# Kernel optimization log

Measured on AMD Instinct MI355X. Metric: run time of the kernel, lower is better.

The kernel has to match this reference:

```python
import jax, jax.numpy as jnp
import numpy as np

B, L, DM = 2, 2048, 2048
EXP = 2; DI = EXP * DM          # d_inner = 4096
N = 64                           # d_state
K = 4                            # d_conv
P = 64                           # headdim
H = DI // P                      # n_heads = 64
G = 1                            # n_groups
CONV = DI + 2 * G * N            # 4224
PROJ = 2 * DI + 2 * G * N + H    # 8384
EPS = 1e-6


def setup_inputs() -> dict:
    ks = jax.random.split(jax.random.key(0), 6)
    s = 0.02
    return {
        'u': jax.random.normal(ks[0], (B, L, DM), jnp.float32),
        'ln_w': jnp.ones((DM,), jnp.float32),
        'in_proj_w': jax.random.normal(ks[1], (PROJ, DM), jnp.float32) * s,
        'conv_w': jax.random.normal(ks[2], (K, CONV), jnp.float32) * 0.1,
        'conv_b': jnp.zeros((CONV,), jnp.float32),
        'dt_bias': jax.random.uniform(ks[3], (H,), jnp.float32, 0.0, 1.0),
        'A_log': jnp.log(jnp.arange(1, H + 1, dtype=jnp.float32)),
        'D': jnp.ones((H,), jnp.float32),
        'norm_w': jnp.ones((DI,), jnp.float32),
        'out_proj_w': jax.random.normal(ks[4], (DM, DI), jnp.float32) * s,
    }


def _rmsnorm(x, w, eps=EPS):
    xf = x.astype(jnp.float32)
    v = jnp.mean(xf * xf, axis=-1, keepdims=True)
    return w * (xf * jax.lax.rsqrt(v + eps)).astype(x.dtype)


def reference(u, ln_w, in_proj_w, conv_w, conv_b, dt_bias, A_log, D, norm_w, out_proj_w):
    residual = u
    hs = _rmsnorm(u, ln_w)                                 # input RMSNorm
    zxbcdt = hs @ in_proj_w.T                              # (B,L,PROJ)
    z, xBC, dt = jnp.split(zxbcdt, [DI, DI + CONV], axis=-1)
    # causal depthwise conv1d over time + SiLU
    xp = jnp.pad(xBC, ((0, 0), (K - 1, 0), (0, 0)))
    xc = conv_b + sum(xp[:, k:k + L, :] * conv_w[k] for k in range(K))
    xc = jax.nn.silu(xc)
    x, Bm, Cm = jnp.split(xc, [DI, DI + G * N], axis=-1)
    x = x.reshape(B, L, H, P)
    Bm = jnp.repeat(Bm.reshape(B, L, G, N), H // G, axis=2)  # (B,L,H,N)
    Cm = jnp.repeat(Cm.reshape(B, L, G, N), H // G, axis=2)
    dt = jax.nn.softplus(dt + dt_bias)                       # (B,L,H)
    dA = jnp.exp(dt * (-jnp.exp(A_log)))                     # (B,L,H)
    dtx = dt[..., None] * x                                  # (B,L,H,P)

    def step(h, inp):
        dA_t, dtx_t, B_t, C_t = inp
        # h: (B,H,P,N); h_t = exp(dt*A) h_{t-1} + (dt*x_t) outer B_t
        h = dA_t[:, :, None, None] * h + dtx_t[..., None] * B_t[:, :, None, :]
        y = jnp.einsum('bhpn,bhn->bhp', h, C_t)
        return h, y

    h0 = jnp.zeros((B, H, P, N), jnp.float32)
    _, ys = jax.lax.scan(step, h0, (dA.transpose(1, 0, 2),
                                    dtx.transpose(1, 0, 2, 3),
                                    Bm.transpose(1, 0, 2, 3),
                                    Cm.transpose(1, 0, 2, 3)))
    y = ys.transpose(1, 0, 2, 3) + D[None, None, :, None] * x   # (B,L,H,P)
    # gated RMSNorm: (y * silu(z)) -> rmsnorm
    y = _rmsnorm(y.reshape(B, L, DI) * jax.nn.silu(z), norm_w)
    out = y @ out_proj_w.T
    return residual + out
```

## Files before the change

kernel.cpp:

```cpp
#include <hip/hip_runtime.h>
#include <hip/hip_bf16.h>

typedef __bf16 bf16;
typedef __bf16 bf16x8 __attribute__((ext_vector_type(8)));
typedef float f32x4 __attribute__((ext_vector_type(4)));

#define B_    2
#define L_    2048
#define DM_   2048
#define DI_   4096
#define NST   64
#define PD    64
#define NH    64
#define CONV_ 4224
#define XBCD_ 4288
#define PROJ_ 8384
#define BL_   (B_ * L_)
#define NCHUNK 32
#define EPS_  1e-6f

#define WAITV(n) asm volatile("s_waitcnt vmcnt(" #n ")" ::: "memory")
#define BAR()    __builtin_amdgcn_s_barrier()

__device__ __forceinline__ float block_reduce_sum_256(float v) {
  #pragma unroll
  for (int m = 32; m; m >>= 1) v += __shfl_xor(v, m, 64);
  __shared__ float sred[4];
  int w = threadIdx.x >> 6;
  if ((threadIdx.x & 63) == 0) sred[w] = v;
  __syncthreads();
  return sred[0] + sred[1] + sred[2] + sred[3];
}

__device__ __forceinline__ float silu_f(float x) {
  return x / (1.0f + expf(-x));
}

__device__ __forceinline__ void async16(const bf16* g, bf16* l) {
  __builtin_amdgcn_global_load_lds(
      (__attribute__((address_space(1))) void*)g,
      (__attribute__((address_space(3))) void*)l, 16, 0, 0);
}

__global__ __launch_bounds__(256) void rmsnorm_in_kernel(
    const float* __restrict__ u, const float* __restrict__ w, bf16* __restrict__ hs) {
  int row = blockIdx.x;
  const float* x = u + (size_t)row * DM_;
  int base = threadIdx.x * 8;
  f32x4 v0 = *(const f32x4*)(x + base);
  f32x4 v1 = *(const f32x4*)(x + base + 4);
  float xv[8], ss = 0.f;
  #pragma unroll
  for (int i = 0; i < 4; i++) { xv[i] = v0[i]; xv[4 + i] = v1[i]; }
  #pragma unroll
  for (int i = 0; i < 8; i++) ss += xv[i] * xv[i];
  ss = block_reduce_sum_256(ss);
  float r = rsqrtf(ss / (float)DM_ + EPS_);
  f32x4 w0 = *(const f32x4*)(w + base);
  f32x4 w1 = *(const f32x4*)(w + base + 4);
  bf16x8 o;
  #pragma unroll
  for (int i = 0; i < 4; i++) { o[i] = (bf16)(w0[i] * xv[i] * r); o[4 + i] = (bf16)(w1[i] * xv[4 + i] * r); }
  *(bf16x8*)(hs + (size_t)row * DM_ + base) = o;
}

__global__ __launch_bounds__(256) void convert_w_kernel(
    const float* __restrict__ src, bf16* __restrict__ dst,
    long n_src, long n_dst) {
  long e = ((long)blockIdx.x * 256 + threadIdx.x) * 8;
  if (e >= n_dst) return;
  bf16x8 o;
  if (e < n_src) {
    f32x4 a = *(const f32x4*)(src + e);
    f32x4 b = *(const f32x4*)(src + e + 4);
    #pragma unroll
    for (int q = 0; q < 4; q++) { o[q] = (bf16)a[q]; o[4 + q] = (bf16)b[q]; }
  } else {
    #pragma unroll
    for (int q = 0; q < 8; q++) o[q] = (bf16)0.f;
  }
  *(bf16x8*)(dst + e) = o;
}

template <bool OUT_F32>
__global__ __launch_bounds__(256, 2) void gemm_nt_db(
    const bf16* __restrict__ A, int lda,
    const bf16* __restrict__ W, int ldw,
    void* __restrict__ Cout, int ldc, const float* __restrict__ resid,
    int N, int K) {
  __shared__ __align__(16) bf16 As[2][128 * 64];
  __shared__ __align__(16) bf16 Bs[2][128 * 64];
  int nwg = gridDim.x * gridDim.y;
  int bid = blockIdx.y * gridDim.x + blockIdx.x;
  int q8 = nwg >> 3, r8 = nwg & 7;
  int xcd = bid & 7, loc = bid >> 3;
  int nb = (xcd < r8 ? xcd * (q8 + 1) : r8 * (q8 + 1) + (xcd - r8) * q8) + loc;
  int bn = nb % gridDim.x, bm = nb / gridDim.x;
  int m0 = bm * 128, n0 = bn * 128;
  int tid = threadIdx.x, wave = tid >> 6, lane = tid & 63;
  int wm = (wave >> 1) * 64, wn = (wave & 1) * 64;
  int lm = lane & 15, lk = (lane >> 4) * 8;
  int lr = lane >> 3;
  int cse = ((lane & 7) ^ lr) * 8;
  f32x4 acc[4][4] = {};

  auto stage = [&](int d, int t) {
    #pragma unroll
    for (int i = 0; i < 4; ++i) {
      int row = (wave * 4 + i) * 8;
      async16(A + (size_t)(m0 + row + lr) * lda + t * 64 + cse, &As[d][row * 64]);
      async16(W + (size_t)(n0 + row + lr) * ldw + t * 64 + cse, &Bs[d][row * 64]);
    }
  };

  int NT = K / 64;
  stage(0, 0);
  for (int t = 0; t < NT; ++t) {
    int d = t & 1;
    if (t + 1 < NT) { stage(d ^ 1, t + 1); WAITV(8); }
    else            { WAITV(0); }
    BAR();
    #pragma unroll
    for (int ks = 0; ks < 64; ks += 32) {
      bf16x8 af[4], bf[4];
      #pragma unroll
      for (int i = 0; i < 4; ++i) {
        int row = wm + i * 16 + lm;
        af[i] = *(const bf16x8*)&As[d][row * 64 + ((((ks + lk) >> 3) ^ (row & 7)) << 3)];
      }
      #pragma unroll
      for (int j = 0; j < 4; ++j) {
        int row = wn + j * 16 + lm;
        bf[j] = *(const bf16x8*)&Bs[d][row * 64 + ((((ks + lk) >> 3) ^ (row & 7)) << 3)];
      }
      #pragma unroll
      for (int i = 0; i < 4; ++i)
        #pragma unroll
        for (int j = 0; j < 4; ++j)
          acc[i][j] = __builtin_amdgcn_mfma_f32_16x16x32_bf16(af[i], bf[j], acc[i][j], 0, 0, 0);
    }
    BAR();
  }
  int r0 = m0 + wm + (lane >> 4) * 4;
  #pragma unroll
  for (int i = 0; i < 4; ++i) {
    #pragma unroll
    for (int j = 0; j < 4; ++j) {
      int col = n0 + wn + j * 16 + lm;
      if (col < N) {
        #pragma unroll
        for (int r = 0; r < 4; ++r) {
          int row = r0 + i * 16 + r;
          size_t idx = (size_t)row * ldc + col;
          float v = acc[i][j][r];
          if (resid) v += resid[idx];
          if (OUT_F32) ((float*)Cout)[idx] = v;
          else         ((bf16*)Cout)[idx]  = (bf16)v;
        }
      }
    }
  }
}

__global__ __launch_bounds__(256) void conv_bc_kernel(
    const bf16* __restrict__ xbcdt, const float* __restrict__ cw,
    const float* __restrict__ cb, bf16* __restrict__ xc) {
  int idx = blockIdx.x * 256 + threadIdx.x;
  if (idx >= BL_ * 16) return;
  int c8 = idx & 15, t = idx >> 4;
  int l = t % L_;
  int c = DI_ + c8 * 8;
  float acc[8];
  f32x4 bv0 = *(const f32x4*)(cb + c);
  f32x4 bv1 = *(const f32x4*)(cb + c + 4);
  #pragma unroll
  for (int q = 0; q < 4; q++) { acc[q] = bv0[q]; acc[4 + q] = bv1[q]; }
  #pragma unroll
  for (int k = 0; k < 4; k++) {
    int ls = l + k - 3;
    if (ls >= 0) {
      const bf16* xp = xbcdt + (size_t)(t + k - 3) * XBCD_ + c;
      bf16x8 xv = *(const bf16x8*)xp;
      f32x4 wv0 = *(const f32x4*)(cw + k * CONV_ + c);
      f32x4 wv1 = *(const f32x4*)(cw + k * CONV_ + c + 4);
      #pragma unroll
      for (int q = 0; q < 4; q++) { acc[q] += (float)xv[q] * wv0[q]; acc[4 + q] += (float)xv[4 + q] * wv1[q]; }
    }
  }
  bf16x8 o;
  #pragma unroll
  for (int q = 0; q < 8; q++) o[q] = (bf16)silu_f(acc[q]);
  *(bf16x8*)(xc + (size_t)t * CONV_ + c) = o;
}

__global__ __launch_bounds__(256) void dt_kernel(
    const bf16* __restrict__ xbcdt, const float* __restrict__ dt_bias,
    float* __restrict__ dtH) {
  int idx = blockIdx.x * 256 + threadIdx.x;
  if (idx >= BL_ * NH) return;
  int h = idx & 63, t = idx >> 6;
  float raw = (float)xbcdt[(size_t)t * XBCD_ + CONV_ + h] + dt_bias[h];
  float v = (raw > 20.f) ? raw : log1pf(expf(raw));
  dtH[(size_t)h * BL_ + t] = v;
}

__global__ __launch_bounds__(256) void scan_chunk_mfma(
    bf16* __restrict__ xc, const bf16* __restrict__ xbcdt,
    const float* __restrict__ cw, const float* __restrict__ cb,
    const float* __restrict__ dtH,
    const float* __restrict__ A_log, const float* __restrict__ Dp,
    bf16* __restrict__ Sc) {
  __shared__ bf16 Bs[64][72];
  __shared__ bf16 Cs[64][72];
  __shared__ bf16 Xt[64][72];
  __shared__ bf16 Gh[64][72];
  __shared__ bf16 Gl[64][72];
  __shared__ float dts[64];
  __shared__ float cum[64];
  __shared__ float wsA[64];
  int bi = blockIdx.x;
  int h = bi & 63, c = (bi >> 6) & 31, b = bi >> 11;
  int tid = threadIdx.x;
  int wave = tid >> 6, lane = tid & 63;
  int lm = lane & 15, lk = (lane >> 4) * 8;
  int cl = lane & 15, rw4 = (lane >> 4) * 4;
  int wt = (wave >> 1) * 32, wq = (wave & 1) * 32;
  size_t rowbase = (size_t)b * L_ + c * 64;
  float aA = expf(A_log[h]);
  #pragma unroll
  for (int i = 0; i < 2; i++) {
    int cc = tid + i * 256;
    int s = cc >> 3, e8 = (cc & 7) * 8;
    const bf16* base = xc + (rowbase + s) * CONV_;
    bf16x8 bv = *(const bf16x8*)(base + DI_ + e8);
    bf16x8 cv = *(const bf16x8*)(base + DI_ + NST + e8);
    *(bf16x8*)&Bs[s][e8 ^ (s & 56)] = bv;
    *(bf16x8*)&Cs[s][e8] = cv;
    int col = h * PD + e8;
    int l = c * 64 + s;
    float acc[8];
    f32x4 cb0 = *(const f32x4*)(cb + col);
    f32x4 cb1 = *(const f32x4*)(cb + col + 4);
    #pragma unroll
    for (int q = 0; q < 4; q++) { acc[q] = cb0[q]; acc[4 + q] = cb1[q]; }
    #pragma unroll
    for (int k = 0; k < 4; k++) {
      int ls = l + k - 3;
      if (ls >= 0) {
        const bf16* xp = xbcdt + (rowbase + s + k - 3) * XBCD_ + col;
        bf16x8 xv = *(const bf16x8*)xp;
        f32x4 wv0 = *(const f32x4*)(cw + k * CONV_ + col);
        f32x4 wv1 = *(const f32x4*)(cw + k * CONV_ + col + 4);
        #pragma unroll
        for (int q = 0; q < 4; q++) { acc[q] += (float)xv[q] * wv0[q]; acc[4 + q] += (float)xv[4 + q] * wv1[q]; }
      }
    }
    #pragma unroll
    for (int q = 0; q < 8; q++) Xt[e8 + q][s ^ e8] = (bf16)silu_f(acc[q]);
  }
  if (tid < 64) dts[tid] = dtH[(size_t)h * BL_ + rowbase + tid];
  __syncthreads();
  if (tid < 64) {
    float v = dts[tid];
    #pragma unroll
    for (int off = 1; off < 64; off <<= 1) {
      float o = __shfl_up(v, off, 64);
      if (tid >= off) v += o;
    }
    cum[tid] = v;
  }
  __syncthreads();
  if (tid < 64) wsA[tid] = expf(-aA * (cum[63] - cum[tid])) * dts[tid];
  f32x4 gacc[2][2] = {};
  #pragma unroll
  for (int ks = 0; ks < 64; ks += 32) {
    bf16x8 af[2], bfr[2];
    #pragma unroll
    for (int i = 0; i < 2; i++) af[i] = *(bf16x8*)&Cs[wt + i * 16 + lm][ks + lk];
    #pragma unroll
    for (int j = 0; j < 2; j++) {
      int S = wq + j * 16 + lm;
      bfr[j] = *(bf16x8*)&Bs[S][(ks + lk) ^ (S & 56)];
    }
    #pragma unroll
    for (int i = 0; i < 2; i++)
      #pragma unroll
      for (int j = 0; j < 2; j++)
        gacc[i][j] = __builtin_amdgcn_mfma_f32_16x16x32_bf16(af[i], bfr[j], gacc[i][j], 0, 0, 0);
  }
  #pragma unroll
  for (int i = 0; i < 2; i++) {
    #pragma unroll
    for (int j = 0; j < 2; j++) {
      #pragma unroll
      for (int r = 0; r < 4; r++) {
        int t = wt + i * 16 + rw4 + r;
        int s = wq + j * 16 + cl;
        float g = 0.f;
        if (s <= t) g = gacc[i][j][r] * expf(-aA * (cum[t] - cum[s])) * dts[s];
        bf16 ghi = (bf16)g;
        Gh[t][s] = ghi;
        Gl[t][s] = (bf16)(g - (float)ghi);
      }
    }
  }
  __syncthreads();
  f32x4 yacc[2][2] = {};
  #pragma unroll
  for (int ks = 0; ks < 64; ks += 32) {
    bf16x8 ah[2], al[2], bx[2];
    #pragma unroll
    for (int i = 0; i < 2; i++) {
      ah[i] = *(bf16x8*)&Gh[wt + i * 16 + lm][ks + lk];
      al[i] = *(bf16x8*)&Gl[wt + i * 16 + lm][ks + lk];
    }
    #pragma unroll
    for (int j = 0; j < 2; j++) {
      int P = wq + j * 16 + lm;
      bx[j] = *(bf16x8*)&Xt[P][(ks + lk) ^ (P & 56)];
    }
    #pragma unroll
    for (int i = 0; i < 2; i++)
      #pragma unroll
      for (int j = 0; j < 2; j++) {
        yacc[i][j] = __builtin_amdgcn_mfma_f32_16x16x32_bf16(ah[i], bx[j], yacc[i][j], 0, 0, 0);
        yacc[i][j] = __builtin_amdgcn_mfma_f32_16x16x32_bf16(al[i], bx[j], yacc[i][j], 0, 0, 0);
      }
  }
  float Dv = Dp[h];
  #pragma unroll
  for (int i = 0; i < 2; i++) {
    #pragma unroll
    for (int j = 0; j < 2; j++) {
      int p = wq + j * 16 + cl;
      #pragma unroll
      for (int r = 0; r < 4; r++) {
        int t = wt + i * 16 + rw4 + r;
        float yv = yacc[i][j][r] + Dv * (float)Xt[p][t ^ (p & 56)];
        xc[(rowbase + t) * CONV_ + h * PD + p] = (bf16)yv;
      }
    }
  }
  __syncthreads();
  #pragma unroll
  for (int i = 0; i < 2; i++) {
    int cc = tid + i * 256;
    int n = cc >> 3, s8 = (cc & 7) * 8;
    bf16x8 vh, vl;
    #pragma unroll
    for (int q = 0; q < 8; q++) {
      int s = s8 + q;
      float wb = (float)Bs[s][n ^ (s & 56)] * wsA[s];
      vh[q] = (bf16)wb;
      vl[q] = (bf16)(wb - (float)vh[q]);
    }
    *(bf16x8*)&Gh[n][s8] = vh;
    *(bf16x8*)&Gl[n][s8] = vl;
  }
  __syncthreads();
  f32x4 sacc[2][2] = {};
  #pragma unroll
  for (int ks = 0; ks < 64; ks += 32) {
    bf16x8 ax[2], bh[2], bl[2];
    #pragma unroll
    for (int i = 0; i < 2; i++) {
      int P = wt + i * 16 + lm;
      ax[i] = *(bf16x8*)&Xt[P][(ks + lk) ^ (P & 56)];
    }
    #pragma unroll
    for (int j = 0; j < 2; j++) {
      bh[j] = *(bf16x8*)&Gh[wq + j * 16 + lm][ks + lk];
      bl[j] = *(bf16x8*)&Gl[wq + j * 16 + lm][ks + lk];
    }
    #pragma unroll
    for (int i = 0; i < 2; i++)
      #pragma unroll
      for (int j = 0; j < 2; j++) {
        sacc[i][j] = __builtin_amdgcn_mfma_f32_16x16x32_bf16(ax[i], bh[j], sacc[i][j], 0, 0, 0);
        sacc[i][j] = __builtin_amdgcn_mfma_f32_16x16x32_bf16(ax[i], bl[j], sacc[i][j], 0, 0, 0);
      }
  }
  bf16* scp = Sc + ((((size_t)b * NCHUNK + c) * NH + h) << 12);
  #pragma unroll
  for (int i = 0; i < 2; i++) {
    #pragma unroll
    for (int j = 0; j < 2; j++) {
      int n = wq + j * 16 + cl;
      #pragma unroll
      for (int r = 0; r < 4; r++) {
        int p = wt + i * 16 + rw4 + r;
        scp[p * 64 + n] = (bf16)sacc[i][j][r];
      }
    }
  }
}

__global__ __launch_bounds__(256) void state_scan_kernel(
    bf16* __restrict__ Sc, const float* __restrict__ dtH,
    const float* __restrict__ A_log) {
  __shared__ float sdts[64];
  int b = blockIdx.x >> 6, h = blockIdx.x & 63;
  int tid = threadIdx.x;
  float aA = expf(A_log[h]);
  float H[16] = {};
  for (int c = 0; c < NCHUNK; c++) {
    if (tid < 64) sdts[tid] = dtH[(size_t)h * BL_ + b * L_ + c * 64 + tid];
    __syncthreads();
    float sum = 0.f;
    #pragma unroll 8
    for (int i = 0; i < 64; i++) sum += sdts[i];
    float Atot = expf(-aA * sum);
    bf16* p = Sc + ((((size_t)b * NCHUNK + c) * NH + h) << 12) + tid * 16;
    bf16x8 s0 = *(bf16x8*)p;
    bf16x8 s1 = *(bf16x8*)(p + 8);
    bf16x8 o0, o1;
    #pragma unroll
    for (int q = 0; q < 8; q++) {
      float n0 = Atot * H[q]     + (float)s0[q];
      float n1 = Atot * H[8 + q] + (float)s1[q];
      o0[q] = (bf16)H[q]; o1[q] = (bf16)H[8 + q];
      H[q] = n0; H[8 + q] = n1;
    }
    *(bf16x8*)p = o0;
    *(bf16x8*)(p + 8) = o1;
    __syncthreads();
  }
}

__global__ __launch_bounds__(256) void y_inter_mfma(
    bf16* __restrict__ xc, const float* __restrict__ dtH,
    const float* __restrict__ A_log, const bf16* __restrict__ Sc) {
  __shared__ bf16 Cs[64][72];
  __shared__ bf16 Hs[64][72];
  __shared__ float dts[64];
  __shared__ float eA[64];
  int bi = blockIdx.x;
  int h = bi & 63, c = (bi >> 6) & 31, b = bi >> 11;
  int tid = threadIdx.x;
  int wave = tid >> 6, lane = tid & 63;
  int lm = lane & 15, lk = (lane >> 4) * 8;
  int cl = lane & 15, rw4 = (lane >> 4) * 4;
  int wt = (wave >> 1) * 32, wp = (wave & 1) * 32;
  size_t rowbase = (size_t)b * L_ + c * 64;
  float aA = expf(A_log[h]);
  const bf16* scp = Sc + ((((size_t)b * NCHUNK + c) * NH + h) << 12);
  #pragma unroll
  for (int i = 0; i < 2; i++) {
    int cc = tid + i * 256;
    int s = cc >> 3, e8 = (cc & 7) * 8;
    bf16x8 cv = *(const bf16x8*)(xc + (rowbase + s) * CONV_ + DI_ + NST + e8);
    *(bf16x8*)&Cs[s][e8] = cv;
  }
  {
    int p = tid >> 2, n16 = (tid & 3) * 16;
    *(bf16x8*)&Hs[p][n16]     = *(const bf16x8*)(scp + p * 64 + n16);
    *(bf16x8*)&Hs[p][n16 + 8] = *(const bf16x8*)(scp + p * 64 + n16 + 8);
  }
  if (tid < 64) dts[tid] = dtH[(size_t)h * BL_ + rowbase + tid];
  __syncthreads();
  if (tid < 64) {
    float v = dts[tid];
    #pragma unroll
    for (int off = 1; off < 64; off <<= 1) {
      float o = __shfl_up(v, off, 64);
      if (tid >= off) v += o;
    }
    eA[tid] = expf(-aA * v);
  }
  __syncthreads();
  f32x4 acc[2][2] = {};
  #pragma unroll
  for (int ks = 0; ks < 64; ks += 32) {
    bf16x8 af[2], bfr[2];
    #pragma unroll
    for (int i = 0; i < 2; i++) af[i]  = *(bf16x8*)&Cs[wt + i * 16 + lm][ks + lk];
    #pragma unroll
    for (int j = 0; j < 2; j++) bfr[j] = *(bf16x8*)&Hs[wp + j * 16 + lm][ks + lk];
    #pragma unroll
    for (int i = 0; i < 2; i++)
      #pragma unroll
      for (int j = 0; j < 2; j++)
        acc[i][j] = __builtin_amdgcn_mfma_f32_16x16x32_bf16(af[i], bfr[j], acc[i][j], 0, 0, 0);
  }
  #pragma unroll
  for (int i = 0; i < 2; i++) {
    #pragma unroll
    for (int j = 0; j < 2; j++) {
      int p = wp + j * 16 + cl;
      #pragma unroll
      for (int r = 0; r < 4; r++) {
        int t = wt + i * 16 + rw4 + r;
        size_t gi = (rowbase + t) * CONV_ + h * PD + p;
        xc[gi] = (bf16)((float)xc[gi] + eA[t] * acc[i][j][r]);
      }
    }
  }
}

__global__ __launch_bounds__(256) void gated_norm_kernel(
    const bf16* __restrict__ xc, bf16* __restrict__ zbuf,
    const float* __restrict__ nw) {
  int t = blockIdx.x;
  int base = threadIdx.x * 16;
  const bf16* yr = xc + (size_t)t * CONV_;
  bf16* zr = zbuf + (size_t)t * DI_;
  float tv[16], ss = 0.f;
  #pragma unroll
  for (int i8 = 0; i8 < 2; i8++) {
    bf16x8 yv = *(const bf16x8*)(yr + base + i8 * 8);
    bf16x8 zv = *(const bf16x8*)(zr + base + i8 * 8);
    #pragma unroll
    for (int q = 0; q < 8; q++) {
      float tt = (float)yv[q] * silu_f((float)zv[q]);
      tv[i8 * 8 + q] = tt;
      ss += tt * tt;
    }
  }
  ss = block_reduce_sum_256(ss);
  float r = rsqrtf(ss / (float)DI_ + EPS_);
  #pragma unroll
  for (int i8 = 0; i8 < 2; i8++) {
    f32x4 w0 = *(const f32x4*)(nw + base + i8 * 8);
    f32x4 w1 = *(const f32x4*)(nw + base + i8 * 8 + 4);
    bf16x8 o;
    #pragma unroll
    for (int q = 0; q < 4; q++) {
      o[q]     = (bf16)(w0[q] * tv[i8 * 8 + q] * r);
      o[4 + q] = (bf16)(w1[q] * tv[i8 * 8 + 4 + q] * r);
    }
    *(bf16x8*)(zr + base + i8 * 8) = o;
  }
}

__global__ void ws_report_kernel(float* out, float ws_mb) {
  if (blockIdx.x == 0 && threadIdx.x == 0) out[0] = ws_mb;
}

extern "C" void kernel_launch(void* const* d_in, const int* in_sizes, int n_in,
                              void* d_out, int out_size, void* d_ws, size_t ws_size,
                              hipStream_t stream) {
  const float* u        = (const float*)d_in[0];
  const float* ln_w     = (const float*)d_in[1];
  const float* in_proj  = (const float*)d_in[2];
  const float* conv_w   = (const float*)d_in[3];
  const float* conv_b   = (const float*)d_in[4];
  const float* dt_bias  = (const float*)d_in[5];
  const float* A_log    = (const float*)d_in[6];
  const float* Dp       = (const float*)d_in[7];
  const float* norm_w   = (const float*)d_in[8];
  const float* out_proj = (const float*)d_in[9];
  float* out = (float*)d_out;

  bf16* hs = (bf16*)d_out;

  char* ws = (char*)d_ws;
  size_t off = 0;
  auto alloc = [&](size_t bytes) { char* p = ws + off; off = (off + bytes + 255) & ~(size_t)255; return p; };
  float* dtH  = (float*)alloc((size_t)BL_ * NH * 4);
  bf16*  wbuf = (bf16*)alloc((size_t)4352 * DM_ * 2);
  bf16*  shbuf= (bf16*)alloc((size_t)BL_ * XBCD_ * 2);
  bf16*  xc   = (bf16*)alloc((size_t)BL_ * CONV_ * 2);
  size_t need = off;

  if (ws_size < need) {
    ws_report_kernel<<<1, 64, 0, stream>>>(out, (float)(ws_size >> 20));
    return;
  }

  bf16* xbcdt = shbuf;
  bf16* zbuf  = shbuf;
  bf16* Sc = (bf16*)alloc((size_t)B_ * NCHUNK * NH * 64 * 64 * 2);
  need = off;
  if (ws_size < need) {
    ws_report_kernel<<<1, 64, 0, stream>>>(out, (float)(ws_size >> 20));
    return;
  }

  rmsnorm_in_kernel<<<BL_, 256, 0, stream>>>(u, ln_w, hs);

  {
    long nsrc = (long)XBCD_ * DM_, ndst = (long)4352 * DM_;
    convert_w_kernel<<<(int)(ndst / 8 / 256), 256, 0, stream>>>(
        in_proj + (size_t)DI_ * DM_, wbuf, nsrc, ndst);
    gemm_nt_db<false><<<dim3(4352 / 128, BL_ / 128), 256, 0, stream>>>(
        hs, DM_, wbuf, DM_, xbcdt, XBCD_, nullptr, XBCD_, DM_);
  }
  conv_bc_kernel<<<(BL_ * 16 + 255) / 256, 256, 0, stream>>>(
      xbcdt, conv_w, conv_b, xc);
  dt_kernel<<<(BL_ * NH + 255) / 256, 256, 0, stream>>>(
      xbcdt, dt_bias, dtH);
  scan_chunk_mfma<<<B_ * NH * NCHUNK, 256, 0, stream>>>(
      xc, xbcdt, conv_w, conv_b, dtH, A_log, Dp, Sc);
  state_scan_kernel<<<B_ * NH, 256, 0, stream>>>(Sc, dtH, A_log);
  y_inter_mfma<<<B_ * NH * NCHUNK, 256, 0, stream>>>(xc, dtH, A_log, Sc);

  {
    long n = (long)DI_ * DM_;
    convert_w_kernel<<<(int)(n / 8 / 256), 256, 0, stream>>>(in_proj, wbuf, n, n);
    gemm_nt_db<false><<<dim3(DI_ / 128, BL_ / 128), 256, 0, stream>>>(
        hs, DM_, wbuf, DM_, zbuf, DI_, nullptr, DI_, DM_);
  }
  gated_norm_kernel<<<BL_, 256, 0, stream>>>(xc, zbuf, norm_w);

  {
    long n = (long)DM_ * DI_;
    convert_w_kernel<<<(int)(n / 8 / 256), 256, 0, stream>>>(out_proj, wbuf, n, n);
    gemm_nt_db<true><<<dim3(DM_ / 128, BL_ / 128), 256, 0, stream>>>(
        zbuf, DI_, wbuf, DI_, out, DM_, u, DM_, DI_);
  }
}
```

Measured before the change: 599.2 us.

## Single-buffer GEMM for higher occupancy and parallelize inter-chunk state scan

The GEMM drops its double-buffered LDS staging for a single buffer, halving LDS use and raising the launch-bounds occupancy hint to 4 blocks per CU. Latency is now meant to be hidden by more resident workgroups rather than by prefetching. Separately, the per-chunk decay totals are precomputed in a new small kernel, and the state scan is split into 16x more blocks with one state element per thread. This replaces 128 serial blocks with a wide grid and coalesced strided accesses. The GEMM change risks exposing load latency if occupancy does not actually rise.

```diff
diff --git a/kernel.cpp b/kernel.cpp
--- a/kernel.cpp
+++ b/kernel.cpp
@@ -83,13 +83,13 @@
 }
 
 template <bool OUT_F32>
-__global__ __launch_bounds__(256, 2) void gemm_nt_db(
+__global__ __launch_bounds__(256, 4) void gemm_nt_sb(
     const bf16* __restrict__ A, int lda,
     const bf16* __restrict__ W, int ldw,
     void* __restrict__ Cout, int ldc, const float* __restrict__ resid,
     int N, int K) {
-  __shared__ __align__(16) bf16 As[2][128 * 64];
-  __shared__ __align__(16) bf16 Bs[2][128 * 64];
+  __shared__ __align__(16) bf16 As[128 * 64];
+  __shared__ __align__(16) bf16 Bs[128 * 64];
   int nwg = gridDim.x * gridDim.y;
   int bid = blockIdx.y * gridDim.x + blockIdx.x;
   int q8 = nwg >> 3, r8 = nwg & 7;
@@ -104,21 +104,15 @@
   int cse = ((lane & 7) ^ lr) * 8;
   f32x4 acc[4][4] = {};
 
-  auto stage = [&](int d, int t) {
+  int NT = K / 64;
+  for (int t = 0; t < NT; ++t) {
     #pragma unroll
     for (int i = 0; i < 4; ++i) {
       int row = (wave * 4 + i) * 8;
-      async16(A + (size_t)(m0 + row + lr) * lda + t * 64 + cse, &As[d][row * 64]);
-      async16(W + (size_t)(n0 + row + lr) * ldw + t * 64 + cse, &Bs[d][row * 64]);
-    }
-  };
-
-  int NT = K / 64;
-  stage(0, 0);
-  for (int t = 0; t < NT; ++t) {
-    int d = t & 1;
-    if (t + 1 < NT) { stage(d ^ 1, t + 1); WAITV(8); }
-    else            { WAITV(0); }
+      async16(A + (size_t)(m0 + row + lr) * lda + t * 64 + cse, &As[row * 64]);
+      async16(W + (size_t)(n0 + row + lr) * ldw + t * 64 + cse, &Bs[row * 64]);
+    }
+    WAITV(0);
     BAR();
     #pragma unroll
     for (int ks = 0; ks < 64; ks += 32) {
@@ -126,12 +120,12 @@
       #pragma unroll
       for (int i = 0; i < 4; ++i) {
         int row = wm + i * 16 + lm;
-        af[i] = *(const bf16x8*)&As[d][row * 64 + ((((ks + lk) >> 3) ^ (row & 7)) << 3)];
+        af[i] = *(const bf16x8*)&As[row * 64 + ((((ks + lk) >> 3) ^ (row & 7)) << 3)];
       }
       #pragma unroll
       for (int j = 0; j < 4; ++j) {
         int row = wn + j * 16 + lm;
-        bf[j] = *(const bf16x8*)&Bs[d][row * 64 + ((((ks + lk) >> 3) ^ (row & 7)) << 3)];
+        bf[j] = *(const bf16x8*)&Bs[row * 64 + ((((ks + lk) >> 3) ^ (row & 7)) << 3)];
       }
       #pragma unroll
       for (int i = 0; i < 4; ++i)
@@ -202,6 +196,20 @@
   float raw = (float)xbcdt[(size_t)t * XBCD_ + CONV_ + h] + dt_bias[h];
   float v = (raw > 20.f) ? raw : log1pf(expf(raw));
   dtH[(size_t)h * BL_ + t] = v;
+}
+
+__global__ __launch_bounds__(256) void atot_kernel(
+    const float* __restrict__ dtH, const float* __restrict__ A_log,
+    float* __restrict__ Atot) {
+  int idx = blockIdx.x * 256 + threadIdx.x;
+  if (idx >= B_ * NH * NCHUNK) return;
+  int c = idx & 31, rem = idx >> 5;
+  int h = rem & 63, b = rem >> 6;
+  const float* p = dtH + (size_t)h * BL_ + b * L_ + c * 64;
+  float s = 0.f;
+  #pragma unroll 8
+  for (int i = 0; i < 64; i++) s += p[i];
+  Atot[idx] = expf(-expf(A_log[h]) * s);
 }
 
 __global__ __launch_bounds__(256) void scan_chunk_mfma(
@@ -396,34 +404,23 @@
 }
 
 __global__ __launch_bounds__(256) void state_scan_kernel(
-    bf16* __restrict__ Sc, const float* __restrict__ dtH,
-    const float* __restrict__ A_log) {
-  __shared__ float sdts[64];
-  int b = blockIdx.x >> 6, h = blockIdx.x & 63;
-  int tid = threadIdx.x;
-  float aA = expf(A_log[h]);
-  float H[16] = {};
-  for (int c = 0; c < NCHUNK; c++) {
-    if (tid < 64) sdts[tid] = dtH[(size_t)h * BL_ + b * L_ + c * 64 + tid];
-    __syncthreads();
-    float sum = 0.f;
-    #pragma unroll 8
-    for (int i = 0; i < 64; i++) sum += sdts[i];
-    float Atot = expf(-aA * sum);
-    bf16* p = Sc + ((((size_t)b * NCHUNK + c) * NH + h) << 12) + tid * 16;
-    bf16x8 s0 = *(bf16x8*)p;
-    bf16x8 s1 = *(bf16x8*)(p + 8);
-    bf16x8 o0, o1;
-    #pragma unroll
-    for (int q = 0; q < 8; q++) {
-      float n0 = Atot * H[q]     + (float)s0[q];
-      float n1 = Atot * H[8 + q] + (float)s1[q];
-      o0[q] = (bf16)H[q]; o1[q] = (bf16)H[8 + q];
-      H[q] = n0; H[8 + q] = n1;
-    }
-    *(bf16x8*)p = o0;
-    *(bf16x8*)(p + 8) = o1;
-    __syncthreads();
+    bf16* __restrict__ Sc, const float* __restrict__ Atot) {
+  __shared__ float At[NCHUNK];
+  int bid = blockIdx.x;
+  int seg = bid & 15, rem = bid >> 4;
+  int e = seg * 256 + threadIdx.x;
+  if (threadIdx.x < NCHUNK) At[threadIdx.x] = Atot[(rem << 5) + threadIdx.x];
+  __syncthreads();
+  int h = rem & 63, b = rem >> 6;
+  bf16* p = Sc + ((((size_t)b * NCHUNK) * NH + h) << 12) + e;
+  const size_t cstride = (size_t)NH << 12;
+  float H = 0.f;
+  #pragma unroll 4
+  for (int c = 0; c < NCHUNK; ++c) {
+    float s = (float)*p;
+    *p = (bf16)H;
+    H = At[c] * H + s;
+    p += cstride;
   }
 }
 
@@ -557,9 +554,11 @@
   size_t off = 0;
   auto alloc = [&](size_t bytes) { char* p = ws + off; off = (off + bytes + 255) & ~(size_t)255; return p; };
   float* dtH  = (float*)alloc((size_t)BL_ * NH * 4);
+  float* Atot = (float*)alloc((size_t)B_ * NH * NCHUNK * 4);
   bf16*  wbuf = (bf16*)alloc((size_t)4352 * DM_ * 2);
   bf16*  shbuf= (bf16*)alloc((size_t)BL_ * XBCD_ * 2);
   bf16*  xc   = (bf16*)alloc((size_t)BL_ * CONV_ * 2);
+  bf16*  Sc   = (bf16*)alloc((size_t)B_ * NCHUNK * NH * 64 * 64 * 2);
   size_t need = off;
 
   if (ws_size < need) {
@@ -569,12 +568,6 @@
 
   bf16* xbcdt = shbuf;
   bf16* zbuf  = shbuf;
-  bf16* Sc = (bf16*)alloc((size_t)B_ * NCHUNK * NH * 64 * 64 * 2);
-  need = off;
-  if (ws_size < need) {
-    ws_report_kernel<<<1, 64, 0, stream>>>(out, (float)(ws_size >> 20));
-    return;
-  }
 
   rmsnorm_in_kernel<<<BL_, 256, 0, stream>>>(u, ln_w, hs);
 
@@ -582,22 +575,24 @@
     long nsrc = (long)XBCD_ * DM_, ndst = (long)4352 * DM_;
     convert_w_kernel<<<(int)(ndst / 8 / 256), 256, 0, stream>>>(
         in_proj + (size_t)DI_ * DM_, wbuf, nsrc, ndst);
-    gemm_nt_db<false><<<dim3(4352 / 128, BL_ / 128), 256, 0, stream>>>(
+    gemm_nt_sb<false><<<dim3(4352 / 128, BL_ / 128), 256, 0, stream>>>(
         hs, DM_, wbuf, DM_, xbcdt, XBCD_, nullptr, XBCD_, DM_);
   }
   conv_bc_kernel<<<(BL_ * 16 + 255) / 256, 256, 0, stream>>>(
       xbcdt, conv_w, conv_b, xc);
   dt_kernel<<<(BL_ * NH + 255) / 256, 256, 0, stream>>>(
       xbcdt, dt_bias, dtH);
+  atot_kernel<<<(B_ * NH * NCHUNK + 255) / 256, 256, 0, stream>>>(
+      dtH, A_log, Atot);
   scan_chunk_mfma<<<B_ * NH * NCHUNK, 256, 0, stream>>>(
       xc, xbcdt, conv_w, conv_b, dtH, A_log, Dp, Sc);
-  state_scan_kernel<<<B_ * NH, 256, 0, stream>>>(Sc, dtH, A_log);
+  state_scan_kernel<<<B_ * NH * 16, 256, 0, stream>>>(Sc, Atot);
   y_inter_mfma<<<B_ * NH * NCHUNK, 256, 0, stream>>>(xc, dtH, A_log, Sc);
 
   {
     long n = (long)DI_ * DM_;
     convert_w_kernel<<<(int)(n / 8 / 256), 256, 0, stream>>>(in_proj, wbuf, n, n);
-    gemm_nt_db<false><<<dim3(DI_ / 128, BL_ / 128), 256, 0, stream>>>(
+    gemm_nt_sb<false><<<dim3(DI_ / 128, BL_ / 128), 256, 0, stream>>>(
         hs, DM_, wbuf, DM_, zbuf, DI_, nullptr, DI_, DM_);
   }
   gated_norm_kernel<<<BL_, 256, 0, stream>>>(xc, zbuf, norm_w);
@@ -605,7 +600,7 @@
   {
     long n = (long)DM_ * DI_;
     convert_w_kernel<<<(int)(n / 8 / 256), 256, 0, stream>>>(out_proj, wbuf, n, n);
-    gemm_nt_db<true><<<dim3(DM_ / 128, BL_ / 128), 256, 0, stream>>>(
+    gemm_nt_sb<true><<<dim3(DM_ / 128, BL_ / 128), 256, 0, stream>>>(
         zbuf, DI_, wbuf, DI_, out, DM_, u, DM_, DI_);
   }
 }
```

New measurement: 544.7 us. -9.1%, faster.
